# Optimization experiments

Hardware: AMD Instinct MI355X
Metric: run time of the kernel (lower is better)

Reference implementation:

```python
import jax, jax.numpy as jnp
import numpy as np

BANDWIDTH = 1.0


def setup_inputs() -> dict:
    key = jax.random.key(0)
    k1, k2, k3 = jax.random.split(key, 3)
    test_Xs = jax.random.normal(k1, (2048, 64), dtype=jnp.float32)
    train_Xs = jax.random.normal(k2, (4096, 64), dtype=jnp.float32)
    weights = jax.random.uniform(k3, (4096,), dtype=jnp.float32)
    return {"test_Xs": test_Xs, "train_Xs": train_Xs, "weights": weights}


def reference(test_Xs, train_Xs, weights):
    # Gaussian KDE: log p(x_i) = logsumexp_j( -0.5 * ||w_j (x_i - y_j) / h||^2 - Z )
    # Since w_j is a scalar per train point, ||w_j (x_i - y_j)||^2 = w_j^2 * ||x_i - y_j||^2,
    # so we compute pairwise squared distances via the GEMM expansion instead of
    # materializing the [n_test, n_train, d] diff tensor.
    n, d = train_Xs.shape
    h = jnp.float32(BANDWIDTH)
    Z = 0.5 * d * jnp.log(2.0 * jnp.float32(np.pi)) + d * jnp.log(h) + jnp.log(jnp.float32(n))

    test_sq = jnp.sum(test_Xs * test_Xs, axis=-1, keepdims=True)        # [nt, 1]
    train_sq = jnp.sum(train_Xs * train_Xs, axis=-1)[None, :]           # [1, ntr]
    cross = jnp.einsum("td,nd->tn", test_Xs, train_Xs)                  # [nt, ntr]
    dist2 = test_sq - 2.0 * cross + train_sq                            # [nt, ntr]
    dist2 = jnp.maximum(dist2, 0.0)

    scale = (weights / h) ** 2                                           # [ntr]
    log_exp = -0.5 * dist2 * scale[None, :]                              # [nt, ntr]
    return jax.nn.logsumexp(log_exp - Z, axis=-1)                        # [nt]
```

## Files before the change

### kernel.cpp

```cpp
#include <hip/hip_runtime.h>
#include <hip/hip_bf16.h>
#include <math.h>

typedef __attribute__((ext_vector_type(8))) short short8;
typedef __attribute__((ext_vector_type(4))) short short4v;
typedef __attribute__((ext_vector_type(4))) float f32x4;

#define LOG2E 1.44269504088896340736f

__device__ __forceinline__ short bf16bits(float x) {
    __hip_bfloat16 b = __float2bfloat16(x);
    short r;
    __builtin_memcpy(&r, &b, 2);
    return r;
}

__global__ __launch_bounds__(256) void kde_prep(
    const float* __restrict__ testX, const float* __restrict__ trainX,
    const float* __restrict__ w,
    __hip_bfloat16* __restrict__ testbf, __hip_bfloat16* __restrict__ trainbf,
    float* __restrict__ sqx, float2* __restrict__ snh,
    int n_test, int n_train)
{
    const int tid  = threadIdx.x;
    const int wid  = blockIdx.x * 4 + (tid >> 6);
    const int lane = tid & 63;
    const int sub  = lane >> 4;
    const int q    = lane & 15;
    const int row  = wid * 4 + sub;
    if (row >= n_test + n_train) return;

    const float* src;
    __hip_bfloat16* dst;
    int r_local;
    if (row < n_test) { src = testX;  dst = testbf;  r_local = row; }
    else              { src = trainX; dst = trainbf; r_local = row - n_test; }

    const float4 v = ((const float4*)src)[r_local * 16 + q];
    short4v b = { bf16bits(v.x), bf16bits(v.y), bf16bits(v.z), bf16bits(v.w) };
    *(short4v*)(dst + r_local * 64 + q * 4) = b;

    float s = v.x * v.x + v.y * v.y + v.z * v.z + v.w * v.w;
    #pragma unroll
    for (int m = 1; m < 16; m <<= 1) s += __shfl_xor(s, m);
    if (q == 0) {
        if (row < n_test) sqx[r_local] = s;
        else {
            float ww = w[r_local];
            snh[r_local] = make_float2(s, -0.5f * LOG2E * ww * ww);
        }
    }
}

__global__ __launch_bounds__(1024) void kde_main(
    const __hip_bfloat16* __restrict__ testbf,
    const __hip_bfloat16* __restrict__ trainbf,
    const float* __restrict__ sqx, const float2* __restrict__ snh,
    float* __restrict__ partial, int n_test)
{
    __shared__ float lds[16 * 16];

    const int mbase = blockIdx.x * 16;
    const int cc    = blockIdx.y;
    const int wv    = threadIdx.x >> 6;
    const int lane  = threadIdx.x & 63;
    const int cg    = lane & 15;
    const int kg    = lane >> 4;

    const int arow = mbase + cg;
    const short8 a0 = *(const short8*)(testbf + arow * 64 +      kg * 8);
    const short8 a1 = *(const short8*)(testbf + arow * 64 + 32 + kg * 8);

    float sxr[4];
    #pragma unroll
    for (int r = 0; r < 4; ++r) sxr[r] = sqx[mbase + kg * 4 + r];

    float s[4] = {0.f, 0.f, 0.f, 0.f};
    const int colbase = cc * 1024 + wv * 64;

    #pragma unroll
    for (int step = 0; step < 4; ++step) {
        const int bcol = colbase + step * 16 + cg;
        const short8 b0 = *(const short8*)(trainbf + bcol * 64 +      kg * 8);
        const short8 b1 = *(const short8*)(trainbf + bcol * 64 + 32 + kg * 8);
        const float2 p  = snh[bcol];

        f32x4 acc = {0.f, 0.f, 0.f, 0.f};
        acc = __builtin_amdgcn_mfma_f32_16x16x32_bf16(a0, b0, acc, 0, 0, 0);
        acc = __builtin_amdgcn_mfma_f32_16x16x32_bf16(a1, b1, acc, 0, 0, 0);

        #pragma unroll
        for (int r = 0; r < 4; ++r) {
            float d2 = fmaxf(__builtin_fmaf(-2.0f, acc[r], sxr[r] + p.x), 0.0f);
            s[r] += __builtin_exp2f(d2 * p.y);
        }
    }

    #pragma unroll
    for (int m = 1; m < 16; m <<= 1) {
        #pragma unroll
        for (int r = 0; r < 4; ++r) s[r] += __shfl_xor(s[r], m);
    }
    if (cg == 0) {
        #pragma unroll
        for (int r = 0; r < 4; ++r)
            lds[(kg * 4 + r) * 16 + wv] = s[r];
    }
    __syncthreads();

    if (threadIdx.x < 16) {
        const int r = threadIdx.x;
        float sum = 0.f;
        #pragma unroll
        for (int v = 0; v < 16; ++v) sum += lds[r * 16 + v];
        partial[cc * n_test + mbase + r] = sum;
    }
}

__global__ __launch_bounds__(256) void kde_final(
    const float* __restrict__ partial, float* __restrict__ out,
    float Z, int n_test, int n_cc)
{
    const int i = blockIdx.x * 256 + threadIdx.x;
    if (i >= n_test) return;
    float sum = 0.f;
    for (int c = 0; c < n_cc; ++c) sum += partial[c * n_test + i];
    out[i] = __logf(sum) - Z;
}

extern "C" void kernel_launch(void* const* d_in, const int* in_sizes, int n_in,
                              void* d_out, int out_size, void* d_ws, size_t ws_size,
                              hipStream_t stream) {
    const float* testX  = (const float*)d_in[0];
    const float* trainX = (const float*)d_in[1];
    const float* w      = (const float*)d_in[2];
    float* out = (float*)d_out;

    const int d = 64;
    const int n_test  = in_sizes[0] / d;
    const int n_train = in_sizes[1] / d;
    const int n_cc    = n_train / 1024;

    char* ws = (char*)d_ws;
    size_t off = 0;
    __hip_bfloat16* testbf  = (__hip_bfloat16*)(ws + off); off += (size_t)n_test  * d * 2;
    __hip_bfloat16* trainbf = (__hip_bfloat16*)(ws + off); off += (size_t)n_train * d * 2;
    float*  sqx     = (float*)(ws + off);  off += (size_t)n_test * 4;
    float2* snh     = (float2*)(ws + off); off += (size_t)n_train * 8;
    float*  partial = (float*)(ws + off);  off += (size_t)n_cc * n_test * 4;
    (void)ws_size; (void)n_in; (void)out_size;

    const float Z = 0.5f * d * logf(2.0f * (float)M_PI) + logf((float)n_train);

    const int rows = n_test + n_train;
    kde_prep<<<rows / 16, 256, 0, stream>>>(
        testX, trainX, w, testbf, trainbf, sqx, snh, n_test, n_train);

    dim3 grid(n_test / 16, n_cc);
    kde_main<<<grid, 1024, 0, stream>>>(
        testbf, trainbf, sqx, snh, partial, n_test);

    kde_final<<<(n_test + 255) / 256, 256, 0, stream>>>(
        partial, out, Z, n_test, n_cc);
}
```

Baseline: 24.23 us.

## Fuse bf16 conversion and squared norms into main KDE kernel, drop prep pass

Removes the separate prep kernel. The main kernel now reads fp32 test and train rows directly, converts them to bf16 in registers and computes the squared norms with cross-lane shuffles. This saves a launch and the workspace round trip. In exchange every block redundantly converts and reduces train rows, and global reads of fp32 data double. Block size drops to 512 with 8 column chunks, and n_cc is hardcoded to 8, which only holds when n_train is 4096.

```diff
diff --git a/kernel.cpp b/kernel.cpp
--- a/kernel.cpp
+++ b/kernel.cpp
@@ -3,7 +3,6 @@
 #include <math.h>
 
 typedef __attribute__((ext_vector_type(8))) short short8;
-typedef __attribute__((ext_vector_type(4))) short short4v;
 typedef __attribute__((ext_vector_type(4))) float f32x4;
 
 #define LOG2E 1.44269504088896340736f
@@ -15,50 +14,23 @@
     return r;
 }
 
-__global__ __launch_bounds__(256) void kde_prep(
-    const float* __restrict__ testX, const float* __restrict__ trainX,
-    const float* __restrict__ w,
-    __hip_bfloat16* __restrict__ testbf, __hip_bfloat16* __restrict__ trainbf,
-    float* __restrict__ sqx, float2* __restrict__ snh,
-    int n_test, int n_train)
-{
-    const int tid  = threadIdx.x;
-    const int wid  = blockIdx.x * 4 + (tid >> 6);
-    const int lane = tid & 63;
-    const int sub  = lane >> 4;
-    const int q    = lane & 15;
-    const int row  = wid * 4 + sub;
-    if (row >= n_test + n_train) return;
-
-    const float* src;
-    __hip_bfloat16* dst;
-    int r_local;
-    if (row < n_test) { src = testX;  dst = testbf;  r_local = row; }
-    else              { src = trainX; dst = trainbf; r_local = row - n_test; }
-
-    const float4 v = ((const float4*)src)[r_local * 16 + q];
-    short4v b = { bf16bits(v.x), bf16bits(v.y), bf16bits(v.z), bf16bits(v.w) };
-    *(short4v*)(dst + r_local * 64 + q * 4) = b;
-
-    float s = v.x * v.x + v.y * v.y + v.z * v.z + v.w * v.w;
-    #pragma unroll
-    for (int m = 1; m < 16; m <<= 1) s += __shfl_xor(s, m);
-    if (q == 0) {
-        if (row < n_test) sqx[r_local] = s;
-        else {
-            float ww = w[r_local];
-            snh[r_local] = make_float2(s, -0.5f * LOG2E * ww * ww);
-        }
-    }
+__device__ __forceinline__ short8 cvt8(const float4 u, const float4 v) {
+    short8 r;
+    r[0] = bf16bits(u.x); r[1] = bf16bits(u.y); r[2] = bf16bits(u.z); r[3] = bf16bits(u.w);
+    r[4] = bf16bits(v.x); r[5] = bf16bits(v.y); r[6] = bf16bits(v.z); r[7] = bf16bits(v.w);
+    return r;
 }
 
-__global__ __launch_bounds__(1024) void kde_main(
-    const __hip_bfloat16* __restrict__ testbf,
-    const __hip_bfloat16* __restrict__ trainbf,
-    const float* __restrict__ sqx, const float2* __restrict__ snh,
-    float* __restrict__ partial, int n_test)
+__device__ __forceinline__ float sq8(const float4 u, const float4 v) {
+    return u.x*u.x + u.y*u.y + u.z*u.z + u.w*u.w
+         + v.x*v.x + v.y*v.y + v.z*v.z + v.w*v.w;
+}
+
+__global__ __launch_bounds__(512, 6) void kde_main(
+    const float* __restrict__ testX, const float* __restrict__ trainX,
+    const float* __restrict__ w, float* __restrict__ partial, int n_test)
 {
-    __shared__ float lds[16 * 16];
+    __shared__ float lds[16 * 8];
 
     const int mbase = blockIdx.x * 16;
     const int cc    = blockIdx.y;
@@ -68,22 +40,39 @@
     const int kg    = lane >> 4;
 
     const int arow = mbase + cg;
-    const short8 a0 = *(const short8*)(testbf + arow * 64 +      kg * 8);
-    const short8 a1 = *(const short8*)(testbf + arow * 64 + 32 + kg * 8);
+    const float4 af0 = *(const float4*)(testX + arow * 64 + kg * 8);
+    const float4 af1 = *(const float4*)(testX + arow * 64 + kg * 8 + 4);
+    const float4 af2 = *(const float4*)(testX + arow * 64 + 32 + kg * 8);
+    const float4 af3 = *(const float4*)(testX + arow * 64 + 32 + kg * 8 + 4);
+    const short8 a0 = cvt8(af0, af1);
+    const short8 a1 = cvt8(af2, af3);
+
+    float sx = sq8(af0, af1) + sq8(af2, af3);
+    sx += __shfl_xor(sx, 16);
+    sx += __shfl_xor(sx, 32);
 
     float sxr[4];
     #pragma unroll
-    for (int r = 0; r < 4; ++r) sxr[r] = sqx[mbase + kg * 4 + r];
+    for (int r = 0; r < 4; ++r) sxr[r] = __shfl(sx, kg * 4 + r);
 
     float s[4] = {0.f, 0.f, 0.f, 0.f};
-    const int colbase = cc * 1024 + wv * 64;
+    const int colbase = cc * 512 + wv * 64;
 
     #pragma unroll
     for (int step = 0; step < 4; ++step) {
         const int bcol = colbase + step * 16 + cg;
-        const short8 b0 = *(const short8*)(trainbf + bcol * 64 +      kg * 8);
-        const short8 b1 = *(const short8*)(trainbf + bcol * 64 + 32 + kg * 8);
-        const float2 p  = snh[bcol];
+        const float4 bf0 = *(const float4*)(trainX + bcol * 64 + kg * 8);
+        const float4 bf1 = *(const float4*)(trainX + bcol * 64 + kg * 8 + 4);
+        const float4 bf2 = *(const float4*)(trainX + bcol * 64 + 32 + kg * 8);
+        const float4 bf3 = *(const float4*)(trainX + bcol * 64 + 32 + kg * 8 + 4);
+        const float ww  = w[bcol];
+        const short8 b0 = cvt8(bf0, bf1);
+        const short8 b1 = cvt8(bf2, bf3);
+
+        float sy = sq8(bf0, bf1) + sq8(bf2, bf3);
+        sy += __shfl_xor(sy, 16);
+        sy += __shfl_xor(sy, 32);
+        const float nh = (-0.5f * LOG2E) * ww * ww;
 
         f32x4 acc = {0.f, 0.f, 0.f, 0.f};
         acc = __builtin_amdgcn_mfma_f32_16x16x32_bf16(a0, b0, acc, 0, 0, 0);
@@ -91,8 +80,8 @@
 
         #pragma unroll
         for (int r = 0; r < 4; ++r) {
-            float d2 = fmaxf(__builtin_fmaf(-2.0f, acc[r], sxr[r] + p.x), 0.0f);
-            s[r] += __builtin_exp2f(d2 * p.y);
+            float d2 = fmaxf(__builtin_fmaf(-2.0f, acc[r], sxr[r] + sy), 0.0f);
+            s[r] += __builtin_exp2f(d2 * nh);
         }
     }
 
@@ -104,7 +93,7 @@
     if (cg == 0) {
         #pragma unroll
         for (int r = 0; r < 4; ++r)
-            lds[(kg * 4 + r) * 16 + wv] = s[r];
+            lds[(kg * 4 + r) * 8 + wv] = s[r];
     }
     __syncthreads();
 
@@ -112,7 +101,7 @@
         const int r = threadIdx.x;
         float sum = 0.f;
         #pragma unroll
-        for (int v = 0; v < 16; ++v) sum += lds[r * 16 + v];
+        for (int v = 0; v < 8; ++v) sum += lds[r * 8 + v];
         partial[cc * n_test + mbase + r] = sum;
     }
 }
@@ -139,26 +128,15 @@
     const int d = 64;
     const int n_test  = in_sizes[0] / d;
     const int n_train = in_sizes[1] / d;
-    const int n_cc    = n_train / 1024;
+    const int n_cc    = 8;
 
-    char* ws = (char*)d_ws;
-    size_t off = 0;
-    __hip_bfloat16* testbf  = (__hip_bfloat16*)(ws + off); off += (size_t)n_test  * d * 2;
-    __hip_bfloat16* trainbf = (__hip_bfloat16*)(ws + off); off += (size_t)n_train * d * 2;
-    float*  sqx     = (float*)(ws + off);  off += (size_t)n_test * 4;
-    float2* snh     = (float2*)(ws + off); off += (size_t)n_train * 8;
-    float*  partial = (float*)(ws + off);  off += (size_t)n_cc * n_test * 4;
+    float* partial = (float*)d_ws;
     (void)ws_size; (void)n_in; (void)out_size;
 
     const float Z = 0.5f * d * logf(2.0f * (float)M_PI) + logf((float)n_train);
 
-    const int rows = n_test + n_train;
-    kde_prep<<<rows / 16, 256, 0, stream>>>(
-        testX, trainX, w, testbf, trainbf, sqx, snh, n_test, n_train);
-
     dim3 grid(n_test / 16, n_cc);
-    kde_main<<<grid, 1024, 0, stream>>>(
-        testbf, trainbf, sqx, snh, partial, n_test);
+    kde_main<<<grid, 512, 0, stream>>>(testX, trainX, w, partial, n_test);
 
     kde_final<<<(n_test + 255) / 256, 256, 0, stream>>>(
         partial, out, Z, n_test, n_cc);
```

New measurement: 27.95 us. +15.3%, slower.

## Shrink main blocks to 256 threads and write per-wave partials without LDS

Applied to the files above, without the earlier changes.

The main kernel now uses 256-thread blocks, each covering 256 training columns, instead of 1024-thread blocks. Each wave writes its four row sums straight to global memory as a float4, so the LDS buffer and block-wide barrier are gone. The final kernel then reduces over 64 partial slots instead of 4. This is meant to cut barrier stalls and improve scheduling flexibility, at the cost of a larger partial buffer (about 512 KB) that the final pass must read.

```diff
diff --git a/kernel.cpp b/kernel.cpp
--- a/kernel.cpp
+++ b/kernel.cpp
@@ -52,16 +52,13 @@
     }
 }
 
-__global__ __launch_bounds__(1024) void kde_main(
+__global__ __launch_bounds__(256, 8) void kde_main(
     const __hip_bfloat16* __restrict__ testbf,
     const __hip_bfloat16* __restrict__ trainbf,
     const float* __restrict__ sqx, const float2* __restrict__ snh,
     float* __restrict__ partial, int n_test)
 {
-    __shared__ float lds[16 * 16];
-
     const int mbase = blockIdx.x * 16;
-    const int cc    = blockIdx.y;
     const int wv    = threadIdx.x >> 6;
     const int lane  = threadIdx.x & 63;
     const int cg    = lane & 15;
@@ -76,7 +73,7 @@
     for (int r = 0; r < 4; ++r) sxr[r] = sqx[mbase + kg * 4 + r];
 
     float s[4] = {0.f, 0.f, 0.f, 0.f};
-    const int colbase = cc * 1024 + wv * 64;
+    const int colbase = blockIdx.y * 256 + wv * 64;
 
     #pragma unroll
     for (int step = 0; step < 4; ++step) {
@@ -101,30 +98,23 @@
         #pragma unroll
         for (int r = 0; r < 4; ++r) s[r] += __shfl_xor(s[r], m);
     }
+
     if (cg == 0) {
-        #pragma unroll
-        for (int r = 0; r < 4; ++r)
-            lds[(kg * 4 + r) * 16 + wv] = s[r];
-    }
-    __syncthreads();
-
-    if (threadIdx.x < 16) {
-        const int r = threadIdx.x;
-        float sum = 0.f;
-        #pragma unroll
-        for (int v = 0; v < 16; ++v) sum += lds[r * 16 + v];
-        partial[cc * n_test + mbase + r] = sum;
+        const int slot = blockIdx.y * 4 + wv;
+        float4 v4 = make_float4(s[0], s[1], s[2], s[3]);
+        *(float4*)(partial + (size_t)slot * n_test + mbase + kg * 4) = v4;
     }
 }
 
 __global__ __launch_bounds__(256) void kde_final(
     const float* __restrict__ partial, float* __restrict__ out,
-    float Z, int n_test, int n_cc)
+    float Z, int n_test, int n_slots)
 {
     const int i = blockIdx.x * 256 + threadIdx.x;
     if (i >= n_test) return;
     float sum = 0.f;
-    for (int c = 0; c < n_cc; ++c) sum += partial[c * n_test + i];
+    #pragma unroll 8
+    for (int c = 0; c < n_slots; ++c) sum += partial[(size_t)c * n_test + i];
     out[i] = __logf(sum) - Z;
 }
 
@@ -139,7 +129,7 @@
     const int d = 64;
     const int n_test  = in_sizes[0] / d;
     const int n_train = in_sizes[1] / d;
-    const int n_cc    = n_train / 1024;
+    const int n_slots = (n_train / 256) * 4;
 
     char* ws = (char*)d_ws;
     size_t off = 0;
@@ -147,7 +137,7 @@
     __hip_bfloat16* trainbf = (__hip_bfloat16*)(ws + off); off += (size_t)n_train * d * 2;
     float*  sqx     = (float*)(ws + off);  off += (size_t)n_test * 4;
     float2* snh     = (float2*)(ws + off); off += (size_t)n_train * 8;
-    float*  partial = (float*)(ws + off);  off += (size_t)n_cc * n_test * 4;
+    float*  partial = (float*)(ws + off);  off += (size_t)n_slots * n_test * 4;
     (void)ws_size; (void)n_in; (void)out_size;
 
     const float Z = 0.5f * d * logf(2.0f * (float)M_PI) + logf((float)n_train);
@@ -156,10 +146,10 @@
     kde_prep<<<rows / 16, 256, 0, stream>>>(
         testX, trainX, w, testbf, trainbf, sqx, snh, n_test, n_train);
 
-    dim3 grid(n_test / 16, n_cc);
-    kde_main<<<grid, 1024, 0, stream>>>(
+    dim3 grid(n_test / 16, n_train / 256);
+    kde_main<<<grid, 256, 0, stream>>>(
         testbf, trainbf, sqx, snh, partial, n_test);
 
     kde_final<<<(n_test + 255) / 256, 256, 0, stream>>>(
-        partial, out, Z, n_test, n_cc);
+        partial, out, Z, n_test, n_slots);
 }
```

Measured after the change: 25.84 us. 1.07x slower.
